# Kernel tuning notes

Measured on AMD Instinct MI355X. Metric: run time of the kernel, lower is better.

## Reference

```python
import jax, jax.numpy as jnp
import numpy as np

B, S, D = 2, 2048, 768
H = 12
DEPTH = D // H
DFF = 4 * D
EPS = 1e-5


def setup_inputs() -> dict:
    key = jax.random.key(0)
    ks = jax.random.split(key, 9)
    sd = 0.02
    return {
        "x": jax.random.normal(ks[0], (B, S, D), dtype=jnp.float32),
        "Wqkv": jax.random.normal(ks[1], (D, 3 * D), dtype=jnp.float32) * sd,
        "Wout": jax.random.normal(ks[2], (D, D), dtype=jnp.float32) * sd,
        "bout": jnp.zeros((D,), dtype=jnp.float32),
        "W1": jax.random.normal(ks[3], (D, DFF), dtype=jnp.float32) * sd,
        "b1": jnp.zeros((DFF,), dtype=jnp.float32),
        "W2": jax.random.normal(ks[4], (DFF, D), dtype=jnp.float32) * sd,
        "b2": jnp.zeros((D,), dtype=jnp.float32),
        "g1": jnp.ones((D,), dtype=jnp.float32),
        "be1": jnp.zeros((D,), dtype=jnp.float32),
        "g2": jnp.ones((D,), dtype=jnp.float32),
        "be2": jnp.zeros((D,), dtype=jnp.float32),
    }


def _layernorm(x, gain, bias):
    mean = jnp.mean(x, axis=-1, keepdims=True)
    var = jnp.mean(jnp.square(x - mean), axis=-1, keepdims=True)  # unbiased=False
    return gain * (x - mean) / jnp.sqrt(var + EPS) + bias


def reference(x, Wqkv, Wout, bout, W1, b1, W2, b2, g1, be1, g2, be2):
    b, s, d = x.shape
    # QKV projection (no bias), chunk into q,k,v
    qkv = jnp.einsum("bsd,de->bse", x, Wqkv)
    q, k, v = jnp.split(qkv, 3, axis=-1)
    q = q.reshape(b, s, H, DEPTH).transpose(0, 2, 1, 3)  # bhsd
    k = k.reshape(b, s, H, DEPTH).transpose(0, 2, 1, 3)
    v = v.reshape(b, s, H, DEPTH).transpose(0, 2, 1, 3)
    scores = jnp.einsum("bhqd,bhkd->bhqk", q, k) / np.sqrt(DEPTH).astype(np.float32)
    # causal mask (use_masking=True)
    causal = jnp.tril(jnp.ones((s, s), dtype=bool))
    scores = jnp.where(causal, scores, -jnp.inf)
    attn = jax.nn.softmax(scores, axis=-1)
    ctx = jnp.einsum("bhqk,bhkd->bhqd", attn, v)
    ctx = ctx.transpose(0, 2, 1, 3).reshape(b, s, d)
    attn_out = jnp.einsum("bsd,de->bse", ctx, Wout) + bout
    # residual + LN1 (dropout is identity in eval)
    h = _layernorm(x + attn_out, g1, be1)
    # FFN
    ff = jax.nn.relu(jnp.einsum("bsd,df->bsf", h, W1) + b1)
    ff = jnp.einsum("bsf,fd->bsd", ff, W2) + b2
    return _layernorm(h + ff, g2, be2)
```

## Files before the change

kernel.cpp:

```cpp
#include <hip/hip_runtime.h>


typedef __attribute__((ext_vector_type(8)))  short    short8;
typedef __attribute__((ext_vector_type(4)))  float    floatx4;
typedef __attribute__((ext_vector_type(16))) float    floatx16;
typedef __attribute__((ext_vector_type(4)))  unsigned uint4v;

#define QSC 0.18033688f
#define C2  24.0f

__device__ __forceinline__ float b2f(unsigned short u) {
    return __uint_as_float(((unsigned)u) << 16);
}
__device__ __forceinline__ unsigned short f2b(float f) {
    unsigned x = __float_as_uint(f);
    return (unsigned short)((x + 0x7fffu + ((x >> 16) & 1u)) >> 16);
}
__device__ __forceinline__ void async_cp16(const void* g, void* l) {
    __builtin_amdgcn_global_load_lds((const __attribute__((address_space(1))) void*)g,
                                     (__attribute__((address_space(3))) void*)l,
                                     16, 0, 0);
}
__device__ __forceinline__ unsigned cvtpk(float lo, float hi) {
    unsigned r;
    asm("v_cvt_pk_bf16_f32 %0, %1, %2" : "=v"(r) : "v"(lo), "v"(hi));
    return r;
}
__device__ __forceinline__ void plswap(unsigned& a, unsigned& b) {
    asm("v_permlane32_swap_b32 %0, %1" : "+v"(a), "+v"(b));
}
__device__ __forceinline__ int chunk_ofs8(int qb) {
    int t = qb >> 2, rem = qb & 3;
    return (t + 1) * (2 * t + rem);
}
__device__ __forceinline__ int swz16(int row, int chunk) {
    return row * 64 + (((chunk ^ (row & 7)) & 7) << 3);
}
__device__ __forceinline__ int swzB(int row, int chunk) {
    return row * 64 + (((chunk ^ (row & 7) ^ ((row >> 2) & 6)) & 7) << 3);
}

__global__ __launch_bounds__(256) void prep_all(
    const float* __restrict__ x,    unsigned short* __restrict__ xb,
    const float* __restrict__ Wqkv, unsigned short* __restrict__ wqkvT,
    const float* __restrict__ Wout, unsigned short* __restrict__ woutT,
    const float* __restrict__ W1,   unsigned short* __restrict__ w1T,
    const float* __restrict__ W2,   unsigned short* __restrict__ w2T)
{
    __shared__ float tile[32][33];
    int idx = blockIdx.x;
    int tx = threadIdx.x & 31, ty = threadIdx.x >> 5;
    if (idx >= 6912) {
        int i = (idx - 6912) * 256 + threadIdx.x;
        float4 v = ((const float4*)x)[i];
        ushort4 u;
        u.x = f2b(v.x); u.y = f2b(v.y); u.z = f2b(v.z); u.w = f2b(v.w);
        ((ushort4*)xb)[i] = u;
        return;
    }
    const float* W; unsigned short* Wt; int K, N, bx, by;
    if (idx < 1728)      { W = Wqkv; Wt = wqkvT; K = 768;  N = 2304; bx = idx % 72;        by = idx / 72; }
    else if (idx < 2304) { W = Wout; Wt = woutT; K = 768;  N = 768;  bx = (idx-1728) % 24; by = (idx-1728) / 24; }
    else if (idx < 4608) { W = W1;   Wt = w1T;   K = 768;  N = 3072; bx = (idx-2304) % 96; by = (idx-2304) / 96; }
    else                 { W = W2;   Wt = w2T;   K = 3072; N = 768;  bx = (idx-4608) % 24; by = (idx-4608) / 24; }
    int n0 = bx * 32, k0 = by * 32;
    for (int i = ty; i < 32; i += 8)
        tile[i][tx] = W[(size_t)(k0 + i) * N + n0 + tx];
    __syncthreads();
    for (int i = ty; i < 32; i += 8)
        Wt[(size_t)(n0 + i) * K + k0 + tx] = f2b(tile[tx][i]);
}

__global__ __launch_bounds__(256) void gemm_bf16(
    const unsigned short* __restrict__ A,
    const unsigned short* __restrict__ Bt,
    const float* __restrict__ bias,
    float* __restrict__ outF,
    unsigned short* __restrict__ outB,
    int M, int N, int K, int relu, int mode, int kslab)
{
    __shared__ unsigned short As[8192];
    __shared__ unsigned short Bs[8192];
    const int tid  = threadIdx.x;
    const int m0   = blockIdx.y * 128;
    const int n0   = blockIdx.x * 128;
    const int kz   = blockIdx.z;
    const int kbeg = kz * kslab;
    const int kend = kbeg + kslab;
    const int lane = tid & 63;
    const int wave = tid >> 6;
    const int wm   = (wave >> 1) * 64;
    const int wn   = (wave & 1) * 64;
    const int fr   = lane & 15;
    const int fq   = lane >> 4;

    floatx4 acc[4][4];
    for (int i = 0; i < 4; i++)
        for (int j = 0; j < 4; j++)
            for (int e = 0; e < 4; e++) acc[i][j][e] = 0.f;

    for (int kk = kbeg; kk < kend; kk += 64) {
        __syncthreads();
        #pragma unroll
        for (int r = 0; r < 4; ++r) {
            int c   = r * 256 + tid;
            int row = c >> 3;
            int jj  = ((c & 7) ^ (row & 7)) * 8;
            async_cp16(A  + (size_t)(m0 + row) * K + kk + jj, &As[c * 8]);
            async_cp16(Bt + (size_t)(n0 + row) * K + kk + jj, &Bs[c * 8]);
        }
        __syncthreads();

        #pragma unroll
        for (int kc = 0; kc < 2; ++kc) {
            short8 a[4], b[4];
            #pragma unroll
            for (int t = 0; t < 4; t++) a[t] = *(const short8*)&As[swz16(wm + t * 16 + fr, kc * 4 + fq)];
            #pragma unroll
            for (int t = 0; t < 4; t++) b[t] = *(const short8*)&Bs[swz16(wn + t * 16 + fr, kc * 4 + fq)];
            #pragma unroll
            for (int i = 0; i < 4; i++)
                #pragma unroll
                for (int j = 0; j < 4; j++)
                    acc[i][j] = __builtin_amdgcn_mfma_f32_16x16x32_bf16(a[i], b[j], acc[i][j], 0, 0, 0);
        }
    }

    if (mode == 2) {
        float* dst = outF + (size_t)kz * M * N;
        #pragma unroll
        for (int j = 0; j < 4; j++) {
            int col = n0 + wn + j * 16 + fr;
            #pragma unroll
            for (int i = 0; i < 4; i++) {
                int rbase = m0 + wm + i * 16 + fq * 4;
                #pragma unroll
                for (int e = 0; e < 4; e++)
                    dst[(size_t)(rbase + e) * N + col] = acc[i][j][e];
            }
        }
        return;
    }
    if (mode == 1) {
        #pragma unroll
        for (int j = 0; j < 4; j++) {
            int col   = n0 + wn + j * 16 + fr;
            int which = (col >= 1536) ? 2 : (col >= 768 ? 1 : 0);
            float sc  = (which == 0) ? QSC : 1.0f;
            int rem   = col - which * 768;
            int hh    = rem >> 6, d = rem & 63;
            #pragma unroll
            for (int i = 0; i < 4; i++) {
                int rbase = m0 + wm + i * 16 + fq * 4;
                #pragma unroll
                for (int e = 0; e < 4; e++) {
                    int row = rbase + e;
                    int b_  = row >> 11, srow = row & 2047;
                    size_t idx = (size_t)which * 3145728 +
                                 ((size_t)(b_ * 12 + hh) * 2048 + srow) * 64 + d;
                    outB[idx] = f2b(acc[i][j][e] * sc);
                }
            }
        }
        return;
    }
    #pragma unroll
    for (int j = 0; j < 4; j++) {
        int col  = n0 + wn + j * 16 + fr;
        float bv = bias ? bias[col] : 0.f;
        #pragma unroll
        for (int i = 0; i < 4; i++) {
            int rbase = m0 + wm + i * 16 + fq * 4;
            #pragma unroll
            for (int e = 0; e < 4; e++) {
                float v = acc[i][j][e] + bv;
                if (relu) v = fmaxf(v, 0.f);
                size_t idx = (size_t)(rbase + e) * N + col;
                if (outF) outF[idx] = v;
                if (outB) outB[idx] = f2b(v);
            }
        }
    }
}

__global__ __launch_bounds__(256, 4) void attn_part(const unsigned short* __restrict__ Qg,
                                                    const unsigned short* __restrict__ Kg,
                                                    const unsigned short* __restrict__ Vg,
                                                    unsigned short* __restrict__ pO,
                                                    float* __restrict__ pL) {
    __shared__ unsigned short Ks[2][4096];
    __shared__ unsigned short Vt[2][4096];
    const int tid  = threadIdx.x;
    const int lane = tid & 63;
    const int wave = tid >> 6;
    const int ql   = lane & 31;
    const int hi   = lane >> 5;
    const int wm   = wave * 32;
    const int bid  = blockIdx.y * 40 + blockIdx.x;
    const int swz  = (bid & 7) * 120 + (bid >> 3);
    const int bh   = swz / 40;
    const int r    = 39 - (swz % 40);
    int qb = 0;
    for (int q_ = 15; q_ >= 0; --q_) if (r >= chunk_ofs8(q_)) { qb = q_; break; }
    const int c     = r - chunk_ofs8(qb);
    const int q0    = qb * 128;
    const int tile0 = 8 * c;
    const int ntk   = min(8, 2 * (qb + 1) - 8 * c);
    const int slot  = bh * 40 + r;
    const unsigned short* Qb = Qg + (size_t)bh * 131072;
    const unsigned short* Kb = Kg + (size_t)bh * 131072;
    const unsigned short* Vb = Vg + (size_t)bh * 131072;
    const int qrow = q0 + wm + ql;

    short8 qf[4];
    {
        const unsigned short* qr = Qb + (size_t)qrow * 64 + hi * 8;
        #pragma unroll
        for (int c4 = 0; c4 < 4; ++c4)
            qf[c4] = *(const short8*)(qr + c4 * 16);
    }

    floatx16 o[2];
    #pragma unroll
    for (int db = 0; db < 2; ++db)
        #pragma unroll
        for (int e = 0; e < 16; ++e) o[db][e] = 0.f;
    float ls[4] = {0.f, 0.f, 0.f, 0.f};

    const int c0 = tid, c1 = tid + 256;
    uint4 kr0, kr1, vr0, vr1;

#define LOADT(TG)                                                              \
    {                                                                          \
        int base = (TG) * 64;                                                  \
        kr0 = *(const uint4*)(Kb + (size_t)(base + (c0 >> 3)) * 64 + (c0 & 7) * 8); \
        kr1 = *(const uint4*)(Kb + (size_t)(base + (c1 >> 3)) * 64 + (c1 & 7) * 8); \
        vr0 = *(const uint4*)(Vb + (size_t)(base + (c0 & 63)) * 64 + (c0 >> 6) * 8); \
        vr1 = *(const uint4*)(Vb + (size_t)(base + (c1 & 63)) * 64 + (c1 >> 6) * 8); \
    }
#define WRITET(BUF)                                                            \
    {                                                                          \
        *(uint4*)&Ks[BUF][swzB(c0 >> 3, c0 & 7)] = kr0;                       \
        *(uint4*)&Ks[BUF][swzB(c1 >> 3, c1 & 7)] = kr1;                       \
        unsigned short t0[8]; *(uint4*)t0 = vr0;                               \
        _Pragma("unroll") for (int i_ = 0; i_ < 8; ++i_) {                     \
            int rv = (c0 >> 6) * 8 + i_;                                       \
            Vt[BUF][rv * 64 + (((((c0 >> 3) & 7) ^ i_ ^ ((rv >> 2) & 6)) & 7) << 3) + (c0 & 7)] = t0[i_]; \
        }                                                                      \
        unsigned short t1[8]; *(uint4*)t1 = vr1;                               \
        _Pragma("unroll") for (int i_ = 0; i_ < 8; ++i_) {                     \
            int rv = (c1 >> 6) * 8 + i_;                                       \
            Vt[BUF][rv * 64 + (((((c1 >> 3) & 7) ^ i_ ^ ((rv >> 2) & 6)) & 7) << 3) + (c1 & 7)] = t1[i_]; \
        }                                                                      \
    }

    LOADT(tile0);
    WRITET(0);
    __syncthreads();

    for (int kt = 0; kt < ntk; ++kt) {
        const int  tg   = tile0 + kt;
        const int  cur  = kt & 1;
        const bool more = (kt + 1 < ntk);
        if (more) LOADT(tg + 1);

        #pragma unroll
        for (int bb = 0; bb < 2; ++bb) {
            short8 kf[4];
            #pragma unroll
            for (int c4 = 0; c4 < 4; ++c4)
                kf[c4] = *(const short8*)&Ks[cur][swzB(32 * bb + ql, 2 * c4 + hi)];
            floatx16 s;
            #pragma unroll
            for (int e = 0; e < 16; ++e) s[e] = 0.f;
            #pragma unroll
            for (int c4 = 0; c4 < 4; ++c4)
                s = __builtin_amdgcn_mfma_f32_32x32x16_bf16(kf[c4], qf[c4], s, 0, 0, 0);

            const int  kvb = tg * 64 + 32 * bb + 4 * hi;
            const bool nm  = (tg * 64 + 32 * bb + 31) > (q0 + wm);
            if (nm) {
                #pragma unroll
                for (int e = 0; e < 16; ++e)
                    if (kvb + (e & 3) + 8 * (e >> 2) > qrow) s[e] = -1e30f;
            }
            float pv[16];
            #pragma unroll
            for (int e = 0; e < 16; ++e) {
                pv[e] = __builtin_amdgcn_exp2f(s[e] - C2);
                ls[e & 3] += pv[e];
            }

            unsigned w[8];
            #pragma unroll
            for (int m = 0; m < 4; ++m) {
                w[2 * m]     = cvtpk(pv[4 * m],     pv[4 * m + 1]);
                w[2 * m + 1] = cvtpk(pv[4 * m + 2], pv[4 * m + 3]);
            }
            plswap(w[0], w[2]);
            plswap(w[1], w[3]);
            plswap(w[4], w[6]);
            plswap(w[5], w[7]);
            uint4v u0 = {w[0], w[1], w[2], w[3]};
            uint4v u1 = {w[4], w[5], w[6], w[7]};
            short8 pa0 = __builtin_bit_cast(short8, u0);
            short8 pa1 = __builtin_bit_cast(short8, u1);

            #pragma unroll
            for (int db = 0; db < 2; ++db) {
                short8 vf0 = *(const short8*)&Vt[cur][swzB(32 * db + ql, 4 * bb + hi)];
                short8 vf1 = *(const short8*)&Vt[cur][swzB(32 * db + ql, 4 * bb + 2 + hi)];
                o[db] = __builtin_amdgcn_mfma_f32_32x32x16_bf16(pa0, vf0, o[db], 0, 0, 0);
                o[db] = __builtin_amdgcn_mfma_f32_32x32x16_bf16(pa1, vf1, o[db], 0, 0, 0);
            }
        }

        if (more) {
            WRITET(cur ^ 1);
            __syncthreads();
        }
    }
#undef LOADT
#undef WRITET

    float lsum = (ls[0] + ls[1]) + (ls[2] + ls[3]);
    lsum += __shfl_xor(lsum, 32);

    __syncthreads();
    unsigned short* Ost = &Ks[0][0];
    #pragma unroll
    for (int db = 0; db < 2; ++db)
        #pragma unroll
        for (int e = 0; e < 16; ++e) {
            int row = wm + (e & 3) + 8 * (e >> 2) + 4 * hi;
            int col = db * 32 + ql;
            Ost[row * 64 + ((((col >> 3) ^ (row & 7)) & 7) << 3) + (col & 7)] =
                f2b(o[db][e]);
        }
    __syncthreads();
    #pragma unroll
    for (int p = 0; p < 4; ++p) {
        int chunk = p * 256 + tid;
        int row = chunk >> 3, cc = chunk & 7;
        uint4 val = *(const uint4*)&Ost[row * 64 + (((cc ^ (row & 7)) & 7) << 3)];
        *(uint4*)(pO + ((size_t)slot * 128 + row) * 64 + cc * 8) = val;
    }
    if (lane < 32)
        pL[(size_t)slot * 128 + wm + ql] = lsum;
}

__global__ __launch_bounds__(256) void attn_combine(const unsigned short* __restrict__ pO,
                                                    const float* __restrict__ pL,
                                                    unsigned short* __restrict__ ctx) {
    const int qb  = blockIdx.x;
    const int bh  = blockIdx.y;
    const int b   = bh / 12, h = bh % 12;
    const int nch = (qb >> 2) + 1;
    const int slot0 = bh * 40 + chunk_ofs8(qb);
    const int tid = threadIdx.x;
    const int row = tid >> 1;
    const int col0 = (tid & 1) * 32;

    float L = 0.f;
    for (int i = 0; i < nch; ++i)
        L += pL[(size_t)(slot0 + i) * 128 + row];

    float acc[32];
    #pragma unroll
    for (int j = 0; j < 32; ++j) acc[j] = 0.f;
    for (int i = 0; i < nch; ++i) {
        const unsigned short* p = pO + ((size_t)(slot0 + i) * 128 + row) * 64 + col0;
        #pragma unroll
        for (int v4 = 0; v4 < 4; ++v4) {
            uint4 u = *(const uint4*)(p + v4 * 8);
            unsigned short t[8]; *(uint4*)t = u;
            #pragma unroll
            for (int j = 0; j < 8; ++j) acc[v4 * 8 + j] += b2f(t[j]);
        }
    }
    float inv = 1.f / L;
    unsigned short* orow = ctx + ((size_t)(b * 2048 + qb * 128 + row)) * 768 + h * 64 + col0;
    #pragma unroll
    for (int v4 = 0; v4 < 4; ++v4) {
        unsigned short t[8];
        #pragma unroll
        for (int j = 0; j < 8; ++j) t[j] = f2b(acc[v4 * 8 + j] * inv);
        *(uint4*)(orow + v4 * 8) = *(uint4*)t;
    }
}

__global__ __launch_bounds__(256) void resid_ln2(const float* __restrict__ X,
                                                 const float* __restrict__ P,
                                                 int nsplit,
                                                 const float* __restrict__ bv,
                                                 const float* __restrict__ gain,
                                                 const float* __restrict__ beta,
                                                 float* __restrict__ outF,
                                                 unsigned short* __restrict__ outB) {
    const int row = blockIdx.x;
    const int t   = threadIdx.x;
    const size_t off = (size_t)row * 768;
    float v[3];
    #pragma unroll
    for (int i = 0; i < 3; i++) {
        size_t c = off + t + i * 256;
        float r = X[c] + bv[t + i * 256];
        for (int p = 0; p < nsplit; ++p) r += P[(size_t)p * 3145728 + c];
        v[i] = r;
    }
    float s  = v[0] + v[1] + v[2];
    float s2 = v[0] * v[0] + v[1] * v[1] + v[2] * v[2];
    #pragma unroll
    for (int o2 = 32; o2 > 0; o2 >>= 1) {
        s  += __shfl_down(s,  o2);
        s2 += __shfl_down(s2, o2);
    }
    __shared__ float rs[4], rq[4];
    if ((t & 63) == 0) { rs[t >> 6] = s; rq[t >> 6] = s2; }
    __syncthreads();
    float S    = rs[0] + rs[1] + rs[2] + rs[3];
    float S2   = rq[0] + rq[1] + rq[2] + rq[3];
    float mean = S * (1.0f / 768.0f);
    float var  = S2 * (1.0f / 768.0f) - mean * mean;
    float inv  = rsqrtf(var + 1e-5f);
    #pragma unroll
    for (int i = 0; i < 3; i++) {
        int c   = t + i * 256;
        float y = gain[c] * (v[i] - mean) * inv + beta[c];
        if (outF) outF[off + c] = y;
        if (outB) outB[off + c] = f2b(y);
    }
}

extern "C" void kernel_launch(void* const* d_in, const int* in_sizes, int n_in,
                              void* d_out, int out_size, void* d_ws, size_t ws_size,
                              hipStream_t stream) {
    const float* x    = (const float*)d_in[0];
    const float* Wqkv = (const float*)d_in[1];
    const float* Wout = (const float*)d_in[2];
    const float* bout = (const float*)d_in[3];
    const float* W1   = (const float*)d_in[4];
    const float* b1   = (const float*)d_in[5];
    const float* W2   = (const float*)d_in[6];
    const float* b2   = (const float*)d_in[7];
    const float* g1   = (const float*)d_in[8];
    const float* be1  = (const float*)d_in[9];
    const float* g2   = (const float*)d_in[10];
    const float* be2  = (const float*)d_in[11];
    float* out = (float*)d_out;

    char* ws = (char*)d_ws;
    unsigned short* wqkvT  = (unsigned short*)(ws + 0);
    unsigned short* woutT  = (unsigned short*)(ws + 3538944);
    unsigned short* w1T    = (unsigned short*)(ws + 4718592);
    unsigned short* w2T    = (unsigned short*)(ws + 9437184);
    unsigned short* xb     = (unsigned short*)(ws + 14155776);
    unsigned short* qkvG   = (unsigned short*)(ws + 20447232);
    unsigned short* Qg     = qkvG;
    unsigned short* Kg     = qkvG + 3145728;
    unsigned short* Vg     = qkvG + 6291456;
    unsigned short* pO     = (unsigned short*)(ws + 39321600);
    float*          pL     = (float*)(ws + 67633152);
    unsigned short* ctxb   = (unsigned short*)(ws + 14155776);
    float*          WoutP  = (float*)(ws + 39321600);
    float*          h      = (float*)(ws + 20447232);
    unsigned short* hb     = (unsigned short*)(ws + 77070336);
    unsigned short* ffb    = (unsigned short*)(ws + 39321600);
    float*          W2P    = (float*)(ws + 64487424);

    prep_all<<<9984, 256, 0, stream>>>(x, xb, Wqkv, wqkvT, Wout, woutT, W1, w1T, W2, w2T);
    gemm_bf16<<<dim3(18, 32), 256, 0, stream>>>(xb, wqkvT, nullptr, nullptr, qkvG,
                                                4096, 2304, 768, 0, 1, 768);
    attn_part<<<dim3(40, 24), 256, 0, stream>>>(Qg, Kg, Vg, pO, pL);
    attn_combine<<<dim3(16, 24), 256, 0, stream>>>(pO, pL, ctxb);
    gemm_bf16<<<dim3(6, 32, 3), 256, 0, stream>>>(ctxb, woutT, nullptr, WoutP, nullptr,
                                                  4096, 768, 768, 0, 2, 256);
    resid_ln2<<<4096, 256, 0, stream>>>(x, WoutP, 3, bout, g1, be1, h, hb);
    gemm_bf16<<<dim3(24, 32), 256, 0, stream>>>(hb, w1T, b1, nullptr, ffb,
                                                4096, 3072, 768, 1, 0, 768);
    gemm_bf16<<<dim3(6, 32, 2), 256, 0, stream>>>(ffb, w2T, nullptr, W2P, nullptr,
                                                  4096, 768, 3072, 0, 2, 1536);
    resid_ln2<<<4096, 256, 0, stream>>>(h, W2P, 2, b2, g2, be2, out, nullptr);
}
```

Before: 311.4 us.

## Double-buffer GEMM LDS tiles and remap workgroups across XCDs

The bf16 GEMM now keeps two LDS buffers, so the async global-to-LDS copy of the next K tile is issued before the MFMAs on the current tile run. It also drops one barrier per K iteration. Workgroup IDs are remapped so each XCD gets a contiguous range of output tiles, which is meant to improve L2 reuse of A and B panels. LDS use per block doubles to 64KB, which can lower occupancy.

```diff
diff --git a/kernel.cpp b/kernel.cpp
--- a/kernel.cpp
+++ b/kernel.cpp
@@ -79,11 +79,18 @@
     unsigned short* __restrict__ outB,
     int M, int N, int K, int relu, int mode, int kslab)
 {
-    __shared__ unsigned short As[8192];
-    __shared__ unsigned short Bs[8192];
+    __shared__ unsigned short As[2][8192];
+    __shared__ unsigned short Bs[2][8192];
     const int tid  = threadIdx.x;
-    const int m0   = blockIdx.y * 128;
-    const int n0   = blockIdx.x * 128;
+    const int gx   = gridDim.x;
+    const int nwg  = gx * gridDim.y;
+    const int orig = blockIdx.y * gx + blockIdx.x;
+    const int qch  = nwg >> 3, rem = nwg & 7;
+    const int xcd  = orig & 7, sub = orig >> 3;
+    const int nid  = (xcd < rem ? xcd * (qch + 1)
+                                : rem * (qch + 1) + (xcd - rem) * qch) + sub;
+    const int m0   = (nid / gx) * 128;
+    const int n0   = (nid % gx) * 128;
     const int kz   = blockIdx.z;
     const int kbeg = kz * kslab;
     const int kend = kbeg + kslab;
@@ -99,32 +106,40 @@
         for (int j = 0; j < 4; j++)
             for (int e = 0; e < 4; e++) acc[i][j][e] = 0.f;
 
+#define STAGE(BUF, KK)                                                         \
+    {                                                                          \
+        _Pragma("unroll")                                                      \
+        for (int r_ = 0; r_ < 4; ++r_) {                                       \
+            int c_   = r_ * 256 + tid;       \
+            int row_ = c_ >> 3;                                                \
+            int jj_  = ((c_ & 7) ^ (row_ & 7)) * 8;  \
+            async_cp16(A  + (size_t)(m0 + row_) * K + (KK) + jj_, &As[BUF][c_ * 8]); \
+            async_cp16(Bt + (size_t)(n0 + row_) * K + (KK) + jj_, &Bs[BUF][c_ * 8]); \
+        }                                                                      \
+    }
+
+    STAGE(0, kbeg);
+    __syncthreads();
+    int cur = 0;
     for (int kk = kbeg; kk < kend; kk += 64) {
-        __syncthreads();
-        #pragma unroll
-        for (int r = 0; r < 4; ++r) {
-            int c   = r * 256 + tid;
-            int row = c >> 3;
-            int jj  = ((c & 7) ^ (row & 7)) * 8;
-            async_cp16(A  + (size_t)(m0 + row) * K + kk + jj, &As[c * 8]);
-            async_cp16(Bt + (size_t)(n0 + row) * K + kk + jj, &Bs[c * 8]);
-        }
-        __syncthreads();
-
+        if (kk + 64 < kend) STAGE(cur ^ 1, kk + 64);
         #pragma unroll
         for (int kc = 0; kc < 2; ++kc) {
             short8 a[4], b[4];
             #pragma unroll
-            for (int t = 0; t < 4; t++) a[t] = *(const short8*)&As[swz16(wm + t * 16 + fr, kc * 4 + fq)];
-            #pragma unroll
-            for (int t = 0; t < 4; t++) b[t] = *(const short8*)&Bs[swz16(wn + t * 16 + fr, kc * 4 + fq)];
+            for (int t = 0; t < 4; t++) a[t] = *(const short8*)&As[cur][swz16(wm + t * 16 + fr, kc * 4 + fq)];
+            #pragma unroll
+            for (int t = 0; t < 4; t++) b[t] = *(const short8*)&Bs[cur][swz16(wn + t * 16 + fr, kc * 4 + fq)];
             #pragma unroll
             for (int i = 0; i < 4; i++)
                 #pragma unroll
                 for (int j = 0; j < 4; j++)
                     acc[i][j] = __builtin_amdgcn_mfma_f32_16x16x32_bf16(a[i], b[j], acc[i][j], 0, 0, 0);
         }
-    }
+        __syncthreads();
+        cur ^= 1;
+    }
+#undef STAGE
 
     if (mode == 2) {
         float* dst = outF + (size_t)kz * M * N;
@@ -147,8 +162,8 @@
             int col   = n0 + wn + j * 16 + fr;
             int which = (col >= 1536) ? 2 : (col >= 768 ? 1 : 0);
             float sc  = (which == 0) ? QSC : 1.0f;
-            int rem   = col - which * 768;
-            int hh    = rem >> 6, d = rem & 63;
+            int rem_  = col - which * 768;
+            int hh    = rem_ >> 6, d = rem_ & 63;
             #pragma unroll
             for (int i = 0; i < 4; i++) {
                 int rbase = m0 + wm + i * 16 + fq * 4;
```

New measurement: 302.2 us. 3.0% less time.
